# Performance work log

Hardware: AMD Instinct MI355X
Metric: run time of the kernel (lower is better)

Reference implementation:

```python
import jax, jax.numpy as jnp
import numpy as np

V = 100000
E = 1600000
IN_CH = 128
HEADS = 4
OUT_CH = 16
NEG_SLOPE = 0.2


def setup_inputs() -> dict:
    key = jax.random.key(0)
    k1, k2, k3, k4, k5 = jax.random.split(key, 5)
    x = jax.random.normal(k1, (V, IN_CH), dtype=jnp.float32)
    edge_index = jax.random.randint(k2, (2, E), 0, V, dtype=jnp.int32)
    # Xavier-ish scaled params
    W = jax.random.normal(k3, (IN_CH, HEADS * OUT_CH), dtype=jnp.float32) / np.sqrt(IN_CH)
    a_src = jax.random.normal(k4, (HEADS, OUT_CH), dtype=jnp.float32) / np.sqrt(OUT_CH)
    a_dst = jax.random.normal(k5, (HEADS, OUT_CH), dtype=jnp.float32) / np.sqrt(OUT_CH)
    return {"x": x, "edge_index": edge_index, "W": W, "a_src": a_src, "a_dst": a_dst}


def reference(x, edge_index, W, a_src, a_dst):
    v = x.shape[0]
    h, cout = a_src.shape
    z = (x @ W).reshape(v, h, cout)                      # [V,H,C]
    src, dst = edge_index[0], edge_index[1]
    # per-node attention logits, then gather at edges (same math as gather-then-dot)
    e_src = jnp.einsum("vhc,hc->vh", z, a_src)           # [V,H]
    e_dst = jnp.einsum("vhc,hc->vh", z, a_dst)           # [V,H]
    e = jax.nn.leaky_relu(e_src[src] + e_dst[dst], NEG_SLOPE)  # [E,H]
    # scatter softmax over dst per head
    m = jax.ops.segment_max(e, dst, num_segments=v)      # [V,H]
    # nodes with no incoming edges get -inf max; edges never reference them
    exp_e = jnp.exp(e - m[dst])                          # [E,H]
    denom = jax.ops.segment_sum(exp_e, dst, num_segments=v)  # [V,H]
    alpha = exp_e / (denom[dst] + 1e-9)                  # [E,H]
    # scatter aggregation of weighted source features
    agg = jax.ops.segment_sum(z[src] * alpha[:, :, None], dst, num_segments=v)  # [V,H,C]
    out = jax.nn.elu(agg)
    return out.reshape(v, h * cout)
```

## Files before the change

### kernel.cpp

```cpp
#include <hip/hip_runtime.h>
#include <hip/hip_bf16.h>
#include <cstdint>

#define NV 100000
#define NE 1600000
#define KIN 128
#define NH 4
#define NC 16
#define NF 64
#define NBKT 1563
#define BCAP 1216
#define EPW 16
#define BINWG 196
#define GEMMWG 782
#define NITEMS 978
#define XSTR 136

typedef __attribute__((ext_vector_type(8))) short bf16x8;
typedef __attribute__((ext_vector_type(4))) float f32x4;

__device__ __forceinline__ short f2bf(float f) {
    unsigned u = __float_as_uint(f);
    return (short)((u + 0x7FFFu + ((u >> 16) & 1u)) >> 16);
}

__device__ __forceinline__ unsigned enc11(float w) {
    unsigned t = (__float_as_uint(w) + 0x10000u) >> 17;
    t = min(max(t, 7168u), 9215u);
    return t - 7168u;
}

__global__ __launch_bounds__(512) void k_front(
    const float* __restrict__ x, const float* __restrict__ W,
    const float* __restrict__ a_src, const float* __restrict__ a_dst,
    __hip_bfloat16* __restrict__ z, float* __restrict__ esrc,
    float* __restrict__ edst,
    const int* __restrict__ ei, int* __restrict__ gcur,
    unsigned* __restrict__ barr)
{
    __shared__ union SM {
        struct { int hist[NBKT]; int base[NBKT]; } bin;
        short xs[128 * XSTR];
    } sm;

    const int bi = blockIdx.x;
    const int t = threadIdx.x;

    if (bi % 5 == 0) {
        int* hist = sm.bin.hist;
        int* base = sm.bin.base;
        const int e0 = (bi / 5) * (512 * EPW);

        for (int i = t; i < NBKT; i += 512) hist[i] = 0;
        __syncthreads();

        unsigned pk[EPW];
        short bk[EPW];
#pragma unroll
        for (int i = 0; i < EPW; ++i) {
            const int e = e0 + i * 512 + t;
            if (e < NE) {
                const int s = ei[e];
                const int d = ei[NE + e];
                const int bkt = d >> 6;
                bk[i] = (short)bkt;
                pk[i] = ((unsigned)(d & 63) << 17) | (unsigned)s;
                atomicAdd(&hist[bkt], 1);
            } else {
                bk[i] = -1;
            }
        }
        __syncthreads();
        for (int i = t; i < NBKT; i += 512) {
            const int c = hist[i];
            base[i] = c ? atomicAdd(&gcur[i], c) : 0;
            hist[i] = 0;
        }
        __syncthreads();
#pragma unroll
        for (int i = 0; i < EPW; ++i) {
            if (bk[i] >= 0) {
                const int bkt = bk[i];
                const int pos = base[bkt] + atomicAdd(&hist[bkt], 1);
                if (pos < BCAP)
                    barr[(size_t)bkt * BCAP + pos] = pk[i];
            }
        }
    } else {
        short* xs = sm.xs;
        const int id = bi - bi / 5 - 1;
        const float4* __restrict__ x4 = (const float4*)x;

#pragma unroll
        for (int i = 0; i < 8; ++i) {
            const int li = i * 512 + t;
            const int idx = id * 4096 + li;
            float4 v = make_float4(0.f, 0.f, 0.f, 0.f);
            if (idx < NV * (KIN / 4)) v = x4[idx];
            const unsigned lo = (unsigned)(unsigned short)f2bf(v.x)
                              | ((unsigned)(unsigned short)f2bf(v.y) << 16);
            const unsigned hi = (unsigned)(unsigned short)f2bf(v.z)
                              | ((unsigned)(unsigned short)f2bf(v.w) << 16);
            *(uint2*)&xs[(li >> 5) * XSTR + (li & 31) * 4] = make_uint2(lo, hi);
        }
        __syncthreads();

        const int wv = t >> 6;
        const int lane = t & 63;
        const int n = lane & 15;
        const int quad = lane >> 4;

        bf16x8 bf[16];
#pragma unroll
        for (int ct = 0; ct < 4; ++ct) {
#pragma unroll
            for (int ks = 0; ks < 4; ++ks) {
                bf16x8 f;
#pragma unroll
                for (int j = 0; j < 8; ++j) {
                    const int k = ks * 32 + quad * 8 + j;
                    f[j] = f2bf(W[k * NF + ct * 16 + n]);
                }
                bf[ct * 4 + ks] = f;
            }
        }

        const short* __restrict__ arow = &xs[(wv * 16 + n) * XSTR];
        f32x4 acc[4];
#pragma unroll
        for (int ct = 0; ct < 4; ++ct) acc[ct] = (f32x4){0.f, 0.f, 0.f, 0.f};

#pragma unroll
        for (int ks = 0; ks < 4; ++ks) {
            const bf16x8 af = *(const bf16x8*)(arow + ks * 32 + quad * 8);
#pragma unroll
            for (int ct = 0; ct < 4; ++ct)
                acc[ct] = __builtin_amdgcn_mfma_f32_16x16x32_bf16(
                    af, bf[ct * 4 + ks], acc[ct], 0, 0, 0);
        }

        float as[4], ad[4];
#pragma unroll
        for (int ct = 0; ct < 4; ++ct) {
            as[ct] = a_src[ct * 16 + n];
            ad[ct] = a_dst[ct * 16 + n];
        }
        unsigned short* __restrict__ zz = (unsigned short*)z;
#pragma unroll
        for (int ct = 0; ct < 4; ++ct) {
#pragma unroll
            for (int reg = 0; reg < 4; ++reg) {
                const int r_g = id * 128 + wv * 16 + quad * 4 + reg;
                const float v = acc[ct][reg];
                float ps = v * as[ct];
                float pd = v * ad[ct];
#pragma unroll
                for (int m = 8; m >= 1; m >>= 1) {
                    ps += __shfl_xor(ps, m, 16);
                    pd += __shfl_xor(pd, m, 16);
                }
                if (r_g < NV) {
                    zz[(size_t)r_g * NF + ct * 16 + n] = (unsigned short)f2bf(v);
                    if (n == 0) {
                        esrc[r_g * NH + ct] = ps;
                        edst[r_g * NH + ct] = pd;
                    }
                }
            }
        }
    }
}

__global__ __launch_bounds__(256) void k_back(
    const int* __restrict__ gcur, const unsigned* __restrict__ barr,
    const float* __restrict__ esrc, const float* __restrict__ edst,
    const __hip_bfloat16* __restrict__ z, float* __restrict__ out)
{
    __shared__ __align__(16) unsigned arr[BCAP];
    __shared__ unsigned long long rec[BCAP];
    __shared__ int hist[64], off[64], cur[64];
    __shared__ float4 led[64];
    const int t = threadIdx.x;
    const int b = blockIdx.x;
    int f = gcur[b]; if (f > BCAP) f = BCAP;
    const unsigned* __restrict__ bp = barr + (size_t)b * BCAP;

    if (t < 64) {
        hist[t] = 0;
        cur[t] = 0;
        const int d = b * 64 + t;
        led[t] = (d < NV) ? *(const float4*)(edst + (size_t)d * 4)
                          : make_float4(0.f, 0.f, 0.f, 0.f);
    }
    __syncthreads();
    const int f4 = f >> 2;
    for (int i = t; i < f4; i += 256) {
        const uint4 v = ((const uint4*)bp)[i];
        ((uint4*)arr)[i] = v;
        atomicAdd(&hist[v.x >> 17], 1);
        atomicAdd(&hist[v.y >> 17], 1);
        atomicAdd(&hist[v.z >> 17], 1);
        atomicAdd(&hist[v.w >> 17], 1);
    }
    for (int i = (f4 << 2) + t; i < f; i += 256) {
        const unsigned v = bp[i];
        arr[i] = v;
        atomicAdd(&hist[v >> 17], 1);
    }
    __syncthreads();
    if (t < 64) off[t] = hist[t];
    __syncthreads();
    for (int s = 1; s < 64; s <<= 1) {
        const int v = (t < 64 && t >= s) ? off[t - s] : 0;
        __syncthreads();
        if (t < 64) off[t] += v;
        __syncthreads();
    }
    if (t < 64) off[t] -= hist[t];
    __syncthreads();

    for (int i = t; i < f; i += 256) {
        const unsigned p = arr[i];
        const int dl = p >> 17;
        const unsigned s = p & 0x1FFFFu;
        const int slot = off[dl] + atomicAdd(&cur[dl], 1);
        const float4 e4 = *(const float4*)(esrc + (size_t)s * 4);
        const float4 ed = led[dl];
        float ev;
        ev = e4.x + ed.x; ev = ev > 0.f ? ev : 0.2f * ev;
        const unsigned w0 = enc11(__expf(ev));
        ev = e4.y + ed.y; ev = ev > 0.f ? ev : 0.2f * ev;
        const unsigned w1 = enc11(__expf(ev));
        ev = e4.z + ed.z; ev = ev > 0.f ? ev : 0.2f * ev;
        const unsigned w2 = enc11(__expf(ev));
        ev = e4.w + ed.w; ev = ev > 0.f ? ev : 0.2f * ev;
        const unsigned w3 = enc11(__expf(ev));
        rec[slot] = (unsigned long long)s
            | ((unsigned long long)w0 << 17)
            | ((unsigned long long)w1 << 28)
            | ((unsigned long long)w2 << 39)
            | ((unsigned long long)w3 << 50);
    }
    __syncthreads();

    const int wv = t >> 6;
    const int lane = t & 63;
    const int quad = lane >> 4;
    const int li = lane & 15;
    const int sh = 17 + 11 * (li >> 2);
    const unsigned short* __restrict__ zb = (const unsigned short*)z + li * 4;

    for (int k = 0; k < 16; ++k) {
        const int dl = (k << 2) | wv;
        const int d = b * 64 + dl;
        const int begin = off[dl];
        const int nd = hist[dl];
        float a0 = 0.f, a1 = 0.f, a2 = 0.f, a3 = 0.f, den = 0.f;
        for (int j = 0; j < nd; j += 8) {
            const int je0 = j + quad;
            const int je1 = je0 + 4;
            const unsigned long long r0 = (je0 < nd) ? rec[begin + je0] : 0ull;
            const unsigned long long r1 = (je1 < nd) ? rec[begin + je1] : 0ull;
            const unsigned s0 = (unsigned)r0 & 0x1FFFFu;
            const unsigned s1 = (unsigned)r1 & 0x1FFFFu;
            const float w0 = __uint_as_float(
                ((((unsigned)(r0 >> sh)) & 0x7FFu) + 7168u) << 17);
            const float w1 = __uint_as_float(
                ((((unsigned)(r1 >> sh)) & 0x7FFu) + 7168u) << 17);
            const uint2 zv0 = *(const uint2*)(zb + ((size_t)s0 << 6));
            const uint2 zv1 = *(const uint2*)(zb + ((size_t)s1 << 6));
            a0 = fmaf(w0, __uint_as_float(zv0.x << 16), a0);
            a1 = fmaf(w0, __uint_as_float(zv0.x & 0xFFFF0000u), a1);
            a2 = fmaf(w0, __uint_as_float(zv0.y << 16), a2);
            a3 = fmaf(w0, __uint_as_float(zv0.y & 0xFFFF0000u), a3);
            den += w0;
            a0 = fmaf(w1, __uint_as_float(zv1.x << 16), a0);
            a1 = fmaf(w1, __uint_as_float(zv1.x & 0xFFFF0000u), a1);
            a2 = fmaf(w1, __uint_as_float(zv1.y << 16), a2);
            a3 = fmaf(w1, __uint_as_float(zv1.y & 0xFFFF0000u), a3);
            den += w1;
        }
        a0 += __shfl_xor(a0, 16); a0 += __shfl_xor(a0, 32);
        a1 += __shfl_xor(a1, 16); a1 += __shfl_xor(a1, 32);
        a2 += __shfl_xor(a2, 16); a2 += __shfl_xor(a2, 32);
        a3 += __shfl_xor(a3, 16); a3 += __shfl_xor(a3, 32);
        den += __shfl_xor(den, 16); den += __shfl_xor(den, 32);
        if (lane < 16 && d < NV) {
            const float id = 1.f / (den + 1e-9f);
            float v0 = a0 * id, v1 = a1 * id, v2 = a2 * id, v3 = a3 * id;
            v0 = v0 > 0.f ? v0 : __expf(v0) - 1.f;
            v1 = v1 > 0.f ? v1 : __expf(v1) - 1.f;
            v2 = v2 > 0.f ? v2 : __expf(v2) - 1.f;
            v3 = v3 > 0.f ? v3 : __expf(v3) - 1.f;
            *(float4*)(out + (size_t)d * NF + li * 4) =
                make_float4(v0, v1, v2, v3);
        }
    }
}

extern "C" void kernel_launch(void* const* d_in, const int* in_sizes, int n_in,
                              void* d_out, int out_size, void* d_ws, size_t ws_size,
                              hipStream_t stream)
{
    const float* x     = (const float*)d_in[0];
    const int*   ei    = (const int*)d_in[1];
    const float* W     = (const float*)d_in[2];
    const float* a_src = (const float*)d_in[3];
    const float* a_dst = (const float*)d_in[4];
    float* out = (float*)d_out;

    char* p = (char*)d_ws;
    __hip_bfloat16* z = (__hip_bfloat16*)p;  p += (size_t)NV * NF * 2;
    float* esrc = (float*)p;                 p += (size_t)NV * NH * 4;
    float* edst = (float*)p;                 p += (size_t)NV * NH * 4;
    int*   gcur = (int*)p;                   p += (size_t)NBKT * 4;
    p = (char*)(((uintptr_t)p + 255) & ~(uintptr_t)255);
    unsigned* barr = (unsigned*)p;           p += (size_t)NBKT * BCAP * 4;

    hipMemsetAsync(gcur, 0, (size_t)NBKT * 4, stream);
    k_front<<<NITEMS, 512, 0, stream>>>(x, W, a_src, a_dst, z, esrc, edst,
                                        ei, gcur, barr);
    k_back<<<NBKT, 256, 0, stream>>>(gcur, barr, esrc, edst, z, out);
}
```

Baseline: 180.7 us.

## Interleave z row layout by channel to widen gathers to 16 bytes per lane

The GEMM epilogue now packs the four heads' values for each channel index into one 8-byte store, producing a head-interleaved z row layout. The aggregation kernel uses 8 lanes per row, each loading 16 bytes and holding 8 accumulators across all four heads with per-head denominators. It processes 16 edges per iteration instead of 8 and un-interleaves results through a small shared buffer before a coalesced store. This is meant to cut the number of gather instructions and improve memory efficiency, at the cost of more registers, more shuffles and an extra LDS round trip per node.

```diff
diff --git a/kernel.cpp b/kernel.cpp
--- a/kernel.cpp
+++ b/kernel.cpp
@@ -16,6 +16,7 @@
 #define NITEMS 978
 #define XSTR 136
 
+
 typedef __attribute__((ext_vector_type(8))) short bf16x8;
 typedef __attribute__((ext_vector_type(4))) float f32x4;
 
@@ -28,6 +29,13 @@
     unsigned t = (__float_as_uint(w) + 0x10000u) >> 17;
     t = min(max(t, 7168u), 9215u);
     return t - 7168u;
+}
+
+__device__ __forceinline__ float declo(unsigned u) {
+    return __uint_as_float(u << 16);
+}
+__device__ __forceinline__ float dechi(unsigned u) {
+    return __uint_as_float(u & 0xFFFF0000u);
 }
 
 __global__ __launch_bounds__(512) void k_front(
@@ -139,32 +147,39 @@
                     af, bf[ct * 4 + ks], acc[ct], 0, 0, 0);
         }
 
+        unsigned short* __restrict__ zz = (unsigned short*)z;
+#pragma unroll
+        for (int reg = 0; reg < 4; ++reg) {
+            const int r_g = id * 128 + wv * 16 + quad * 4 + reg;
+            const unsigned lo = (unsigned)(unsigned short)f2bf(acc[0][reg])
+                              | ((unsigned)(unsigned short)f2bf(acc[1][reg]) << 16);
+            const unsigned hi = (unsigned)(unsigned short)f2bf(acc[2][reg])
+                              | ((unsigned)(unsigned short)f2bf(acc[3][reg]) << 16);
+            if (r_g < NV)
+                *(uint2*)(zz + (size_t)r_g * NF + n * 4) = make_uint2(lo, hi);
+        }
+
         float as[4], ad[4];
 #pragma unroll
         for (int ct = 0; ct < 4; ++ct) {
             as[ct] = a_src[ct * 16 + n];
             ad[ct] = a_dst[ct * 16 + n];
         }
-        unsigned short* __restrict__ zz = (unsigned short*)z;
 #pragma unroll
         for (int ct = 0; ct < 4; ++ct) {
 #pragma unroll
             for (int reg = 0; reg < 4; ++reg) {
                 const int r_g = id * 128 + wv * 16 + quad * 4 + reg;
-                const float v = acc[ct][reg];
-                float ps = v * as[ct];
-                float pd = v * ad[ct];
+                float ps = acc[ct][reg] * as[ct];
+                float pd = acc[ct][reg] * ad[ct];
 #pragma unroll
                 for (int m = 8; m >= 1; m >>= 1) {
                     ps += __shfl_xor(ps, m, 16);
                     pd += __shfl_xor(pd, m, 16);
                 }
-                if (r_g < NV) {
-                    zz[(size_t)r_g * NF + ct * 16 + n] = (unsigned short)f2bf(v);
-                    if (n == 0) {
-                        esrc[r_g * NH + ct] = ps;
-                        edst[r_g * NH + ct] = pd;
-                    }
+                if (r_g < NV && n == 0) {
+                    esrc[r_g * NH + ct] = ps;
+                    edst[r_g * NH + ct] = pd;
                 }
             }
         }
@@ -180,6 +195,7 @@
     __shared__ unsigned long long rec[BCAP];
     __shared__ int hist[64], off[64], cur[64];
     __shared__ float4 led[64];
+    __shared__ float obuf[4][64];
     const int t = threadIdx.x;
     const int b = blockIdx.x;
     int f = gcur[b]; if (f > BCAP) f = BCAP;
@@ -245,56 +261,90 @@
 
     const int wv = t >> 6;
     const int lane = t & 63;
-    const int quad = lane >> 4;
-    const int li = lane & 15;
-    const int sh = 17 + 11 * (li >> 2);
-    const unsigned short* __restrict__ zb = (const unsigned short*)z + li * 4;
+    const int q8 = lane >> 3;
+    const int li8 = lane & 7;
+    const unsigned short* __restrict__ zb =
+        (const unsigned short*)z + li8 * 8;
 
     for (int k = 0; k < 16; ++k) {
         const int dl = (k << 2) | wv;
         const int d = b * 64 + dl;
         const int begin = off[dl];
         const int nd = hist[dl];
-        float a0 = 0.f, a1 = 0.f, a2 = 0.f, a3 = 0.f, den = 0.f;
-        for (int j = 0; j < nd; j += 8) {
-            const int je0 = j + quad;
-            const int je1 = je0 + 4;
+        float a0 = 0.f, a1 = 0.f, a2 = 0.f, a3 = 0.f;
+        float a4 = 0.f, a5 = 0.f, a6 = 0.f, a7 = 0.f;
+        float dn0 = 0.f, dn1 = 0.f, dn2 = 0.f, dn3 = 0.f;
+        for (int j = 0; j < nd; j += 16) {
+            const int je0 = j + q8;
+            const int je1 = je0 + 8;
             const unsigned long long r0 = (je0 < nd) ? rec[begin + je0] : 0ull;
             const unsigned long long r1 = (je1 < nd) ? rec[begin + je1] : 0ull;
             const unsigned s0 = (unsigned)r0 & 0x1FFFFu;
             const unsigned s1 = (unsigned)r1 & 0x1FFFFu;
-            const float w0 = __uint_as_float(
-                ((((unsigned)(r0 >> sh)) & 0x7FFu) + 7168u) << 17);
-            const float w1 = __uint_as_float(
-                ((((unsigned)(r1 >> sh)) & 0x7FFu) + 7168u) << 17);
-            const uint2 zv0 = *(const uint2*)(zb + ((size_t)s0 << 6));
-            const uint2 zv1 = *(const uint2*)(zb + ((size_t)s1 << 6));
-            a0 = fmaf(w0, __uint_as_float(zv0.x << 16), a0);
-            a1 = fmaf(w0, __uint_as_float(zv0.x & 0xFFFF0000u), a1);
-            a2 = fmaf(w0, __uint_as_float(zv0.y << 16), a2);
-            a3 = fmaf(w0, __uint_as_float(zv0.y & 0xFFFF0000u), a3);
-            den += w0;
-            a0 = fmaf(w1, __uint_as_float(zv1.x << 16), a0);
-            a1 = fmaf(w1, __uint_as_float(zv1.x & 0xFFFF0000u), a1);
-            a2 = fmaf(w1, __uint_as_float(zv1.y << 16), a2);
-            a3 = fmaf(w1, __uint_as_float(zv1.y & 0xFFFF0000u), a3);
-            den += w1;
-        }
-        a0 += __shfl_xor(a0, 16); a0 += __shfl_xor(a0, 32);
-        a1 += __shfl_xor(a1, 16); a1 += __shfl_xor(a1, 32);
-        a2 += __shfl_xor(a2, 16); a2 += __shfl_xor(a2, 32);
-        a3 += __shfl_xor(a3, 16); a3 += __shfl_xor(a3, 32);
-        den += __shfl_xor(den, 16); den += __shfl_xor(den, 32);
-        if (lane < 16 && d < NV) {
-            const float id = 1.f / (den + 1e-9f);
-            float v0 = a0 * id, v1 = a1 * id, v2 = a2 * id, v3 = a3 * id;
+            const uint4 zv0 = *(const uint4*)(zb + ((size_t)s0 << 6));
+            const uint4 zv1 = *(const uint4*)(zb + ((size_t)s1 << 6));
+            float wA0, wA1, wA2, wA3, wB0, wB1, wB2, wB3;
+            wA0 = __uint_as_float(((((unsigned)(r0 >> 17)) & 0x7FFu) + 7168u) << 17);
+            wA1 = __uint_as_float(((((unsigned)(r0 >> 28)) & 0x7FFu) + 7168u) << 17);
+            wA2 = __uint_as_float(((((unsigned)(r0 >> 39)) & 0x7FFu) + 7168u) << 17);
+            wA3 = __uint_as_float(((((unsigned)(r0 >> 50)) & 0x7FFu) + 7168u) << 17);
+            wB0 = __uint_as_float(((((unsigned)(r1 >> 17)) & 0x7FFu) + 7168u) << 17);
+            wB1 = __uint_as_float(((((unsigned)(r1 >> 28)) & 0x7FFu) + 7168u) << 17);
+            wB2 = __uint_as_float(((((unsigned)(r1 >> 39)) & 0x7FFu) + 7168u) << 17);
+            wB3 = __uint_as_float(((((unsigned)(r1 >> 50)) & 0x7FFu) + 7168u) << 17);
+            a0 = fmaf(wA0, declo(zv0.x), a0);
+            a1 = fmaf(wA1, dechi(zv0.x), a1);
+            a2 = fmaf(wA2, declo(zv0.y), a2);
+            a3 = fmaf(wA3, dechi(zv0.y), a3);
+            a4 = fmaf(wA0, declo(zv0.z), a4);
+            a5 = fmaf(wA1, dechi(zv0.z), a5);
+            a6 = fmaf(wA2, declo(zv0.w), a6);
+            a7 = fmaf(wA3, dechi(zv0.w), a7);
+            dn0 += wA0; dn1 += wA1; dn2 += wA2; dn3 += wA3;
+            a0 = fmaf(wB0, declo(zv1.x), a0);
+            a1 = fmaf(wB1, dechi(zv1.x), a1);
+            a2 = fmaf(wB2, declo(zv1.y), a2);
+            a3 = fmaf(wB3, dechi(zv1.y), a3);
+            a4 = fmaf(wB0, declo(zv1.z), a4);
+            a5 = fmaf(wB1, dechi(zv1.z), a5);
+            a6 = fmaf(wB2, declo(zv1.w), a6);
+            a7 = fmaf(wB3, dechi(zv1.w), a7);
+            dn0 += wB0; dn1 += wB1; dn2 += wB2; dn3 += wB3;
+        }
+#pragma unroll
+        for (int m = 8; m <= 32; m <<= 1) {
+            a0 += __shfl_xor(a0, m); a1 += __shfl_xor(a1, m);
+            a2 += __shfl_xor(a2, m); a3 += __shfl_xor(a3, m);
+            a4 += __shfl_xor(a4, m); a5 += __shfl_xor(a5, m);
+            a6 += __shfl_xor(a6, m); a7 += __shfl_xor(a7, m);
+            dn0 += __shfl_xor(dn0, m); dn1 += __shfl_xor(dn1, m);
+            dn2 += __shfl_xor(dn2, m); dn3 += __shfl_xor(dn3, m);
+        }
+        if (q8 == 0) {
+            const float i0 = 1.f / (dn0 + 1e-9f);
+            const float i1 = 1.f / (dn1 + 1e-9f);
+            const float i2 = 1.f / (dn2 + 1e-9f);
+            const float i3 = 1.f / (dn3 + 1e-9f);
+            float v0 = a0 * i0, v1 = a1 * i1, v2 = a2 * i2, v3 = a3 * i3;
+            float v4 = a4 * i0, v5 = a5 * i1, v6 = a6 * i2, v7 = a7 * i3;
             v0 = v0 > 0.f ? v0 : __expf(v0) - 1.f;
             v1 = v1 > 0.f ? v1 : __expf(v1) - 1.f;
             v2 = v2 > 0.f ? v2 : __expf(v2) - 1.f;
             v3 = v3 > 0.f ? v3 : __expf(v3) - 1.f;
-            *(float4*)(out + (size_t)d * NF + li * 4) =
-                make_float4(v0, v1, v2, v3);
-        }
+            v4 = v4 > 0.f ? v4 : __expf(v4) - 1.f;
+            v5 = v5 > 0.f ? v5 : __expf(v5) - 1.f;
+            v6 = v6 > 0.f ? v6 : __expf(v6) - 1.f;
+            v7 = v7 > 0.f ? v7 : __expf(v7) - 1.f;
+            obuf[wv][0 * 16 + 2 * li8]     = v0;
+            obuf[wv][1 * 16 + 2 * li8]     = v1;
+            obuf[wv][2 * 16 + 2 * li8]     = v2;
+            obuf[wv][3 * 16 + 2 * li8]     = v3;
+            obuf[wv][0 * 16 + 2 * li8 + 1] = v4;
+            obuf[wv][1 * 16 + 2 * li8 + 1] = v5;
+            obuf[wv][2 * 16 + 2 * li8 + 1] = v6;
+            obuf[wv][3 * 16 + 2 * li8 + 1] = v7;
+        }
+        if (d < NV) out[(size_t)d * NF + lane] = obuf[wv][lane];
     }
 }
 
```

Measured after the change: 202.2 us. 1.12x slower.

## Assign one destination per 16-lane group in aggregation; use shuffle-based prefix scan

Applied to the files above, without the earlier changes.

The aggregation loop now gives each 16-lane quarter-wave its own destination node, so each lane walks that node's edges serially and no cross-quad shuffle reduction is needed. Before, a whole wave split one destination's edges across four quads. The 64-entry prefix sum over bucket histograms is replaced by a single-wavefront __shfl_up scan, which removes several block-wide barriers. The trade-off is divergence: within a wave, the four quads handle destinations with different in-degrees, so the loop runs to the largest degree and wave-level memory parallelism per iteration drops.

```diff
diff --git a/kernel.cpp b/kernel.cpp
--- a/kernel.cpp
+++ b/kernel.cpp
@@ -30,6 +30,13 @@
     return t - 7168u;
 }
 
+__device__ __forceinline__ float declo(unsigned u) {
+    return __uint_as_float(u << 16);
+}
+__device__ __forceinline__ float dechi(unsigned u) {
+    return __uint_as_float(u & 0xFFFF0000u);
+}
+
 __global__ __launch_bounds__(512) void k_front(
     const float* __restrict__ x, const float* __restrict__ W,
     const float* __restrict__ a_src, const float* __restrict__ a_dst,
@@ -187,7 +194,6 @@
 
     if (t < 64) {
         hist[t] = 0;
-        cur[t] = 0;
         const int d = b * 64 + t;
         led[t] = (d < NV) ? *(const float4*)(edst + (size_t)d * 4)
                           : make_float4(0.f, 0.f, 0.f, 0.f);
@@ -208,15 +214,17 @@
         atomicAdd(&hist[v >> 17], 1);
     }
     __syncthreads();
-    if (t < 64) off[t] = hist[t];
-    __syncthreads();
-    for (int s = 1; s < 64; s <<= 1) {
-        const int v = (t < 64 && t >= s) ? off[t - s] : 0;
-        __syncthreads();
-        if (t < 64) off[t] += v;
-        __syncthreads();
-    }
-    if (t < 64) off[t] -= hist[t];
+    if (t < 64) {
+        const int h0 = hist[t];
+        int s = h0;
+#pragma unroll
+        for (int m = 1; m < 64; m <<= 1) {
+            const int u = __shfl_up(s, m, 64);
+            if (t >= m) s += u;
+        }
+        off[t] = s - h0;
+        cur[t] = 0;
+    }
     __syncthreads();
 
     for (int i = t; i < f; i += 256) {
@@ -245,47 +253,30 @@
 
     const int wv = t >> 6;
     const int lane = t & 63;
-    const int quad = lane >> 4;
+    const int dstq = lane >> 4;
     const int li = lane & 15;
     const int sh = 17 + 11 * (li >> 2);
     const unsigned short* __restrict__ zb = (const unsigned short*)z + li * 4;
 
-    for (int k = 0; k < 16; ++k) {
-        const int dl = (k << 2) | wv;
+    for (int k = 0; k < 4; ++k) {
+        const int dl = wv * 16 + k * 4 + dstq;
         const int d = b * 64 + dl;
         const int begin = off[dl];
         const int nd = hist[dl];
         float a0 = 0.f, a1 = 0.f, a2 = 0.f, a3 = 0.f, den = 0.f;
-        for (int j = 0; j < nd; j += 8) {
-            const int je0 = j + quad;
-            const int je1 = je0 + 4;
-            const unsigned long long r0 = (je0 < nd) ? rec[begin + je0] : 0ull;
-            const unsigned long long r1 = (je1 < nd) ? rec[begin + je1] : 0ull;
-            const unsigned s0 = (unsigned)r0 & 0x1FFFFu;
-            const unsigned s1 = (unsigned)r1 & 0x1FFFFu;
-            const float w0 = __uint_as_float(
-                ((((unsigned)(r0 >> sh)) & 0x7FFu) + 7168u) << 17);
-            const float w1 = __uint_as_float(
-                ((((unsigned)(r1 >> sh)) & 0x7FFu) + 7168u) << 17);
-            const uint2 zv0 = *(const uint2*)(zb + ((size_t)s0 << 6));
-            const uint2 zv1 = *(const uint2*)(zb + ((size_t)s1 << 6));
-            a0 = fmaf(w0, __uint_as_float(zv0.x << 16), a0);
-            a1 = fmaf(w0, __uint_as_float(zv0.x & 0xFFFF0000u), a1);
-            a2 = fmaf(w0, __uint_as_float(zv0.y << 16), a2);
-            a3 = fmaf(w0, __uint_as_float(zv0.y & 0xFFFF0000u), a3);
-            den += w0;
-            a0 = fmaf(w1, __uint_as_float(zv1.x << 16), a0);
-            a1 = fmaf(w1, __uint_as_float(zv1.x & 0xFFFF0000u), a1);
-            a2 = fmaf(w1, __uint_as_float(zv1.y << 16), a2);
-            a3 = fmaf(w1, __uint_as_float(zv1.y & 0xFFFF0000u), a3);
-            den += w1;
-        }
-        a0 += __shfl_xor(a0, 16); a0 += __shfl_xor(a0, 32);
-        a1 += __shfl_xor(a1, 16); a1 += __shfl_xor(a1, 32);
-        a2 += __shfl_xor(a2, 16); a2 += __shfl_xor(a2, 32);
-        a3 += __shfl_xor(a3, 16); a3 += __shfl_xor(a3, 32);
-        den += __shfl_xor(den, 16); den += __shfl_xor(den, 32);
-        if (lane < 16 && d < NV) {
+        for (int j = 0; j < nd; ++j) {
+            const unsigned long long r = rec[begin + j];
+            const unsigned s = (unsigned)r & 0x1FFFFu;
+            const float w = __uint_as_float(
+                ((((unsigned)(r >> sh)) & 0x7FFu) + 7168u) << 17);
+            const uint2 zv = *(const uint2*)(zb + ((size_t)s << 6));
+            a0 = fmaf(w, declo(zv.x), a0);
+            a1 = fmaf(w, dechi(zv.x), a1);
+            a2 = fmaf(w, declo(zv.y), a2);
+            a3 = fmaf(w, dechi(zv.y), a3);
+            den += w;
+        }
+        if (d < NV) {
             const float id = 1.f / (den + 1e-9f);
             float v0 = a0 * id, v1 = a1 * id, v2 = a2 * id, v3 = a3 * id;
             v0 = v0 > 0.f ? v0 : __expf(v0) - 1.f;
```

New measurement: 177.0 us. 2.0% less time.
